# Kernel tuning notes

Hardware: AMD Instinct MI355X
Metric: run time of the kernel (lower is better)

The kernel has to match this reference:

```python
import jax, jax.numpy as jnp
import numpy as np


def setup_inputs() -> dict:
    key = jax.random.key(0)
    ks = jax.random.split(key, 7)
    B, T, E, H, V = 32, 200, 32, 128, 8000
    s = lambda fan: 1.0 / np.sqrt(fan)
    return {
        "x": jax.random.normal(ks[0], (B, T, E), dtype=jnp.float32),
        "Ww": jax.random.normal(ks[1], (H, H), dtype=jnp.float32) * s(H),
        "Wb": jax.random.normal(ks[2], (H,), dtype=jnp.float32) * s(H),
        "Uw": jax.random.normal(ks[3], (H, E), dtype=jnp.float32) * s(E),
        "Ub": jax.random.normal(ks[4], (H,), dtype=jnp.float32) * s(E),
        "Vw": jax.random.normal(ks[5], (V, H), dtype=jnp.float32) * s(H),
        "Vb": jax.random.normal(ks[6], (V,), dtype=jnp.float32) * s(H),
    }


def reference(x, Ww, Wb, Uw, Ub, Vw, Vb):
    # x: [B, T, E]. Elman RNN: h_t = tanh(W h_{t-1} + b_W + U x_t + b_U); out_t = V h_t + b_V
    B = x.shape[0]
    H = Ww.shape[0]
    h0 = jnp.zeros((B, H), dtype=x.dtype)
    # Precompute input projections for all timesteps at once: [T, B, H]
    ux = jnp.einsum('bte,he->tbh', x, Uw) + Ub + Wb

    def step(h, ux_t):
        h = jnp.tanh(h @ Ww.T + ux_t)
        return h, h

    hidden, hs = jax.lax.scan(step, h0, ux)  # hs: [T, B, H]
    # Output projection applied to all hidden states (same math as per-step V)
    out_seq = jnp.einsum('tbh,vh->btv', hs, Vw) + Vb  # [B, T, V]
    return out_seq, hidden
```

## Files before the change

kernel.cpp:

```cpp
#include <hip/hip_runtime.h>
#include <hip/hip_bf16.h>
#include <stdint.h>

typedef short v8s __attribute__((ext_vector_type(8)));
typedef float v4f __attribute__((ext_vector_type(4)));
typedef float v4fv __attribute__((ext_vector_type(4)));

__device__ __forceinline__ float bf2f(short s) {
    unsigned int u = ((unsigned int)(unsigned short)s) << 16;
    float f;
    __builtin_memcpy(&f, &u, 4);
    return f;
}

__device__ __forceinline__ unsigned short f2bf(float f) {
    unsigned int u;
    __builtin_memcpy(&u, &f, 4);
    unsigned int r = (u + 0x7FFFu + ((u >> 16) & 1u)) >> 16;
    return (unsigned short)r;
}

__device__ __forceinline__ float tanh_fast(float z) {
    float e = __expf(2.0f * z);
    return 1.0f - 2.0f / (e + 1.0f);
}

__global__ __launch_bounds__(256) void ux_kernel(
    const float* __restrict__ x, const float* __restrict__ Uw,
    const float* __restrict__ Ub, const float* __restrict__ Wb,
    float* __restrict__ ux) {
    int row = blockIdx.x * 2 + (threadIdx.x >> 7);
    int i = threadIdx.x & 127;
    int b = row & 31, t = row >> 5;
    const float* xr = x + (b * 200 + t) * 32;
    const float* ur = Uw + i * 32;
    float acc = 0.f;
#pragma unroll
    for (int e4 = 0; e4 < 8; ++e4) {
        v4fv xv = *(const v4fv*)(xr + e4 * 4);
        v4fv uv = *(const v4fv*)(ur + e4 * 4);
#pragma unroll
        for (int j = 0; j < 4; ++j) acc = __builtin_fmaf(xv[j], uv[j], acc);
    }
    ux[row * 128 + i] = acc + Ub[i] + Wb[i];
}

__global__ __launch_bounds__(512) void rnn_kernel(
    const float* __restrict__ Ww, const float* __restrict__ ux,
    short* __restrict__ hs, float* __restrict__ hidden_out) {
    __shared__ alignas(16) short h_hi[2][16][136];
    __shared__ alignas(16) short h_lo[2][16][136];
    const int tid = threadIdx.x;
    const int w = tid >> 6;
    const int lane = tid & 63;
    const int q = lane >> 4, c = lane & 15;
    const int b0 = blockIdx.x * 16;
    const int col = 16 * w + c;

    for (int i = tid; i < 2 * 16 * 136; i += 512) {
        ((short*)h_hi)[i] = 0;
        ((short*)h_lo)[i] = 0;
    }

    v8s w_hi[4], w_lo[4];
#pragma unroll
    for (int kb = 0; kb < 4; ++kb) {
        const float* p = Ww + col * 128 + 32 * kb + 8 * q;
#pragma unroll
        for (int j = 0; j < 8; ++j) {
            float v = p[j];
            unsigned short hi = f2bf(v);
            w_hi[kb][j] = (short)hi;
            w_lo[kb][j] = (short)f2bf(v - bf2f((short)hi));
        }
    }

    float uxv[4];
#pragma unroll
    for (int r = 0; r < 4; ++r)
        uxv[r] = ux[(b0 + 4 * q + r) * 128 + col];

    __syncthreads();

    for (int t = 0; t < 200; ++t) {
        float uxn[4];
        int tn = t < 199 ? t + 1 : 199;
#pragma unroll
        for (int r = 0; r < 4; ++r)
            uxn[r] = ux[(tn * 32 + b0 + 4 * q + r) * 128 + col];

        const int rb = t & 1;
        v4f a0 = {0.f, 0.f, 0.f, 0.f}, a1 = a0, a2 = a0;
#pragma unroll
        for (int kb = 0; kb < 4; ++kb) {
            v8s ahi = *(const v8s*)(&h_hi[rb][c][32 * kb + 8 * q]);
            v8s alo = *(const v8s*)(&h_lo[rb][c][32 * kb + 8 * q]);
            a0 = __builtin_amdgcn_mfma_f32_16x16x32_bf16(ahi, w_hi[kb], a0, 0, 0, 0);
            a1 = __builtin_amdgcn_mfma_f32_16x16x32_bf16(ahi, w_lo[kb], a1, 0, 0, 0);
            a2 = __builtin_amdgcn_mfma_f32_16x16x32_bf16(alo, w_hi[kb], a2, 0, 0, 0);
        }

#pragma unroll
        for (int r = 0; r < 4; ++r) {
            float z = ((a0[r] + a1[r]) + a2[r]) + uxv[r];
            float h = tanh_fast(z);
            unsigned short hh = f2bf(h);
            float rem = h - bf2f((short)hh);
            unsigned short hl = f2bf(rem);
            h_hi[rb ^ 1][4 * q + r][col] = (short)hh;
            h_lo[rb ^ 1][4 * q + r][col] = (short)hl;
            hs[((b0 + 4 * q + r) * 200 + t) * 128 + col] = (short)hh;
            if (t == 199) hidden_out[(b0 + 4 * q + r) * 128 + col] = h;
            uxv[r] = uxn[r];
        }
        __syncthreads();
    }
}

__global__ __launch_bounds__(256) void out_kernel(
    const short* __restrict__ hs, const float* __restrict__ Vw,
    const float* __restrict__ Vb, float* __restrict__ out) {
    const int tid = threadIdx.x;
    const int w = tid >> 6;
    const int lane = tid & 63;
    const int q = lane >> 4, c = lane & 15;
    const int v_wave = blockIdx.x * 128 + 32 * w;
    const int bt0 = blockIdx.y * 128;

    v4f acc[2][8];
#pragma unroll
    for (int a = 0; a < 2; ++a)
#pragma unroll
        for (int b = 0; b < 8; ++b) acc[a][b] = (v4f){0.f, 0.f, 0.f, 0.f};

#pragma unroll
    for (int kb = 0; kb < 4; ++kb) {
        v8s afr[2];
#pragma unroll
        for (int vt = 0; vt < 2; ++vt) {
            int vr = v_wave + 16 * vt + c;
            vr = vr < 8000 ? vr : 7999;
            const float* p = Vw + vr * 128 + 32 * kb + 8 * q;
            v4fv p0 = *(const v4fv*)(p);
            v4fv p1 = *(const v4fv*)(p + 4);
#pragma unroll
            for (int j = 0; j < 4; ++j) {
                afr[vt][j] = (short)f2bf(p0[j]);
                afr[vt][4 + j] = (short)f2bf(p1[j]);
            }
        }
#pragma unroll
        for (int nt = 0; nt < 8; ++nt) {
            v8s bfr = *(const v8s*)(hs + (bt0 + 16 * nt + c) * 128 + 32 * kb + 8 * q);
            acc[0][nt] = __builtin_amdgcn_mfma_f32_16x16x32_bf16(afr[0], bfr, acc[0][nt], 0, 0, 0);
            acc[1][nt] = __builtin_amdgcn_mfma_f32_16x16x32_bf16(afr[1], bfr, acc[1][nt], 0, 0, 0);
        }
    }

#pragma unroll
    for (int vt = 0; vt < 2; ++vt) {
        int v4base = v_wave + 16 * vt + 4 * q;
        bool ok = v4base < 8000;
        int vb_idx = ok ? v4base : 0;
        v4fv vbv = *(const v4fv*)(Vb + vb_idx);
#pragma unroll
        for (int nt = 0; nt < 8; ++nt) {
            long bt = bt0 + 16 * nt + c;
            if (ok) {
                v4fv o;
#pragma unroll
                for (int r = 0; r < 4; ++r) o[r] = acc[vt][nt][r] + vbv[r];
                *(v4fv*)(out + bt * 8000 + v4base) = o;
            }
        }
    }
}

extern "C" void kernel_launch(void* const* d_in, const int* in_sizes, int n_in,
                              void* d_out, int out_size, void* d_ws, size_t ws_size,
                              hipStream_t stream) {
    const float* x  = (const float*)d_in[0];
    const float* Ww = (const float*)d_in[1];
    const float* Wb = (const float*)d_in[2];
    const float* Uw = (const float*)d_in[3];
    const float* Ub = (const float*)d_in[4];
    const float* Vw = (const float*)d_in[5];
    const float* Vb = (const float*)d_in[6];
    float* out = (float*)d_out;

    float* ux = (float*)d_ws;
    short* hs = (short*)((char*)d_ws + 819200 * 4);

    ux_kernel<<<3200, 256, 0, stream>>>(x, Uw, Ub, Wb, ux);
    rnn_kernel<<<2, 512, 0, stream>>>(Ww, ux, hs, out + 51200000);
    dim3 g(63, 50);
    out_kernel<<<g, 256, 0, stream>>>(hs, Vw, Vb, out);
}
```

Baseline: 452.0 us.

## Pre-convert Vw to bf16, streamline RNN step, make hidden states time-major

A separate kernel converts Vw to bf16 once, so the output GEMM no longer converts fp32 per block. The recurrent loop is unrolled by two with precomputed LDS offsets and the bias folded into the accumulator init. It also uses cheaper bf16 rounding (round-half-up, truncate for the low part) and an rcp-based tanh. Hidden states are stored time-major so per-step writes are contiguous, and the output kernel remaps indices to match. The final hidden state is rebuilt from the hi+lo split, which slightly changes precision.

```diff
diff --git a/kernel.cpp b/kernel.cpp
--- a/kernel.cpp
+++ b/kernel.cpp
@@ -1,28 +1,29 @@
 #include <hip/hip_runtime.h>
-#include <hip/hip_bf16.h>
 #include <stdint.h>
 
 typedef short v8s __attribute__((ext_vector_type(8)));
 typedef float v4f __attribute__((ext_vector_type(4)));
-typedef float v4fv __attribute__((ext_vector_type(4)));
 
 __device__ __forceinline__ float bf2f(short s) {
     unsigned int u = ((unsigned int)(unsigned short)s) << 16;
-    float f;
-    __builtin_memcpy(&f, &u, 4);
-    return f;
-}
-
-__device__ __forceinline__ unsigned short f2bf(float f) {
-    unsigned int u;
-    __builtin_memcpy(&u, &f, 4);
-    unsigned int r = (u + 0x7FFFu + ((u >> 16) & 1u)) >> 16;
-    return (unsigned short)r;
-}
-
+    float f; __builtin_memcpy(&f, &u, 4); return f;
+}
+__device__ __forceinline__ unsigned short f2bf_rne(float f) {
+    unsigned int u; __builtin_memcpy(&u, &f, 4);
+    return (unsigned short)((u + 0x7FFFu + ((u >> 16) & 1u)) >> 16);
+}
+__device__ __forceinline__ unsigned short f2bf_rhu(float f) {
+    unsigned int u; __builtin_memcpy(&u, &f, 4);
+    return (unsigned short)((u + 0x8000u) >> 16);
+}
+__device__ __forceinline__ unsigned short f2bf_trunc(float f) {
+    unsigned int u; __builtin_memcpy(&u, &f, 4);
+    return (unsigned short)(u >> 16);
+}
 __device__ __forceinline__ float tanh_fast(float z) {
     float e = __expf(2.0f * z);
-    return 1.0f - 2.0f / (e + 1.0f);
+    float r = __builtin_amdgcn_rcpf(e + 1.0f);
+    return __builtin_fmaf(-2.0f, r, 1.0f);
 }
 
 __global__ __launch_bounds__(256) void ux_kernel(
@@ -37,30 +38,39 @@
     float acc = 0.f;
 #pragma unroll
     for (int e4 = 0; e4 < 8; ++e4) {
-        v4fv xv = *(const v4fv*)(xr + e4 * 4);
-        v4fv uv = *(const v4fv*)(ur + e4 * 4);
+        v4f xv = *(const v4f*)(xr + e4 * 4);
+        v4f uv = *(const v4f*)(ur + e4 * 4);
 #pragma unroll
         for (int j = 0; j < 4; ++j) acc = __builtin_fmaf(xv[j], uv[j], acc);
     }
     ux[row * 128 + i] = acc + Ub[i] + Wb[i];
+}
+
+__global__ __launch_bounds__(256) void vwcvt_kernel(
+    const float* __restrict__ Vw, short* __restrict__ vwb) {
+    int i = (blockIdx.x * 256 + threadIdx.x) * 8;
+    v4f p0 = *(const v4f*)(Vw + i);
+    v4f p1 = *(const v4f*)(Vw + i + 4);
+    v8s o;
+#pragma unroll
+    for (int j = 0; j < 4; ++j) {
+        o[j] = (short)f2bf_rne(p0[j]);
+        o[4 + j] = (short)f2bf_rne(p1[j]);
+    }
+    *(v8s*)(vwb + i) = o;
 }
 
 __global__ __launch_bounds__(512) void rnn_kernel(
     const float* __restrict__ Ww, const float* __restrict__ ux,
     short* __restrict__ hs, float* __restrict__ hidden_out) {
-    __shared__ alignas(16) short h_hi[2][16][136];
-    __shared__ alignas(16) short h_lo[2][16][136];
+    __shared__ alignas(16) short hbuf[2 * 2 * 16 * 136];
+    char* lds = (char*)hbuf;
     const int tid = threadIdx.x;
-    const int w = tid >> 6;
-    const int lane = tid & 63;
-    const int q = lane >> 4, c = lane & 15;
+    const int w = tid >> 6, lane = tid & 63, q = lane >> 4, c = lane & 15;
     const int b0 = blockIdx.x * 16;
     const int col = 16 * w + c;
 
-    for (int i = tid; i < 2 * 16 * 136; i += 512) {
-        ((short*)h_hi)[i] = 0;
-        ((short*)h_lo)[i] = 0;
-    }
+    for (int i = tid; i < 1088; i += 512) ((v8s*)hbuf)[i] = (v8s){0, 0, 0, 0, 0, 0, 0, 0};
 
     v8s w_hi[4], w_lo[4];
 #pragma unroll
@@ -69,63 +79,70 @@
 #pragma unroll
         for (int j = 0; j < 8; ++j) {
             float v = p[j];
-            unsigned short hi = f2bf(v);
+            unsigned short hi = f2bf_rne(v);
             w_hi[kb][j] = (short)hi;
-            w_lo[kb][j] = (short)f2bf(v - bf2f((short)hi));
-        }
-    }
-
-    float uxv[4];
-#pragma unroll
-    for (int r = 0; r < 4; ++r)
-        uxv[r] = ux[(b0 + 4 * q + r) * 128 + col];
+            w_lo[kb][j] = (short)f2bf_rne(v - bf2f((short)hi));
+        }
+    }
+
+    const int rd_base = c * 272 + 16 * q;
+    const int wr_base = q * 1088 + col * 2;
+
+    const float* uxp = ux + (b0 + 4 * q) * 128 + col;
+    float uxv0 = uxp[0], uxv1 = uxp[128], uxv2 = uxp[256], uxv3 = uxp[384];
+    uxp += 4096;
+    short* hsp = hs + (b0 + 4 * q) * 128 + col;
 
     __syncthreads();
 
-    for (int t = 0; t < 200; ++t) {
-        float uxn[4];
-        int tn = t < 199 ? t + 1 : 199;
-#pragma unroll
-        for (int r = 0; r < 4; ++r)
-            uxn[r] = ux[(tn * 32 + b0 + 4 * q + r) * 128 + col];
-
-        const int rb = t & 1;
-        v4f a0 = {0.f, 0.f, 0.f, 0.f}, a1 = a0, a2 = a0;
-#pragma unroll
-        for (int kb = 0; kb < 4; ++kb) {
-            v8s ahi = *(const v8s*)(&h_hi[rb][c][32 * kb + 8 * q]);
-            v8s alo = *(const v8s*)(&h_lo[rb][c][32 * kb + 8 * q]);
-            a0 = __builtin_amdgcn_mfma_f32_16x16x32_bf16(ahi, w_hi[kb], a0, 0, 0, 0);
-            a1 = __builtin_amdgcn_mfma_f32_16x16x32_bf16(ahi, w_lo[kb], a1, 0, 0, 0);
-            a2 = __builtin_amdgcn_mfma_f32_16x16x32_bf16(alo, w_hi[kb], a2, 0, 0, 0);
-        }
-
-#pragma unroll
-        for (int r = 0; r < 4; ++r) {
-            float z = ((a0[r] + a1[r]) + a2[r]) + uxv[r];
-            float h = tanh_fast(z);
-            unsigned short hh = f2bf(h);
-            float rem = h - bf2f((short)hh);
-            unsigned short hl = f2bf(rem);
-            h_hi[rb ^ 1][4 * q + r][col] = (short)hh;
-            h_lo[rb ^ 1][4 * q + r][col] = (short)hl;
-            hs[((b0 + 4 * q + r) * 200 + t) * 128 + col] = (short)hh;
-            if (t == 199) hidden_out[(b0 + 4 * q + r) * 128 + col] = h;
-            uxv[r] = uxn[r];
-        }
-        __syncthreads();
+#define RNN_STEP(RBUF, WBUF)                                                        \
+    {                                                                               \
+        float un0 = uxp[0], un1 = uxp[128], un2 = uxp[256], un3 = uxp[384];         \
+        v4f a0 = {uxv0, uxv1, uxv2, uxv3};                                          \
+        v4f a1 = {0.f, 0.f, 0.f, 0.f}, a2 = a1;                                     \
+        _Pragma("unroll") for (int kb = 0; kb < 4; ++kb) {                          \
+            v8s ahi = *(const v8s*)(lds + (RBUF)*8704 + kb * 64 + rd_base);         \
+            v8s alo = *(const v8s*)(lds + (RBUF)*8704 + 4352 + kb * 64 + rd_base);  \
+            a0 = __builtin_amdgcn_mfma_f32_16x16x32_bf16(ahi, w_hi[kb], a0, 0, 0, 0); \
+            a1 = __builtin_amdgcn_mfma_f32_16x16x32_bf16(ahi, w_lo[kb], a1, 0, 0, 0); \
+            a2 = __builtin_amdgcn_mfma_f32_16x16x32_bf16(alo, w_hi[kb], a2, 0, 0, 0); \
+        }                                                                           \
+        _Pragma("unroll") for (int r = 0; r < 4; ++r) {                             \
+            float z = (a0[r] + a1[r]) + a2[r];                                      \
+            float h = tanh_fast(z);                                                 \
+            unsigned short hh = f2bf_rhu(h);                                        \
+            float rem = h - bf2f((short)hh);                                        \
+            unsigned short hl = f2bf_trunc(rem);                                    \
+            *(short*)(lds + (WBUF)*8704 + r * 272 + wr_base) = (short)hh;           \
+            *(short*)(lds + (WBUF)*8704 + 4352 + r * 272 + wr_base) = (short)hl;    \
+            hsp[r * 128] = (short)hh;                                               \
+        }                                                                           \
+        uxv0 = un0; uxv1 = un1; uxv2 = un2; uxv3 = un3;                             \
+        uxp += 4096; hsp += 4096;                                                   \
+        __syncthreads();                                                            \
+    }
+
+    for (int tp = 0; tp < 100; ++tp) {
+        RNN_STEP(0, 1)
+        RNN_STEP(1, 0)
+    }
+#undef RNN_STEP
+
+#pragma unroll
+    for (int r = 0; r < 4; ++r) {
+        short hh = *(short*)(lds + r * 272 + wr_base);
+        short hl = *(short*)(lds + 4352 + r * 272 + wr_base);
+        hidden_out[(b0 + 4 * q + r) * 128 + col] = bf2f(hh) + bf2f(hl);
     }
 }
 
 __global__ __launch_bounds__(256) void out_kernel(
-    const short* __restrict__ hs, const float* __restrict__ Vw,
+    const short* __restrict__ hs, const short* __restrict__ vwb,
     const float* __restrict__ Vb, float* __restrict__ out) {
     const int tid = threadIdx.x;
-    const int w = tid >> 6;
-    const int lane = tid & 63;
-    const int q = lane >> 4, c = lane & 15;
+    const int w = tid >> 6, lane = tid & 63, q = lane >> 4, c = lane & 15;
     const int v_wave = blockIdx.x * 128 + 32 * w;
-    const int bt0 = blockIdx.y * 128;
+    const int n0 = blockIdx.y * 128;
 
     v4f acc[2][8];
 #pragma unroll
@@ -140,18 +157,11 @@
         for (int vt = 0; vt < 2; ++vt) {
             int vr = v_wave + 16 * vt + c;
             vr = vr < 8000 ? vr : 7999;
-            const float* p = Vw + vr * 128 + 32 * kb + 8 * q;
-            v4fv p0 = *(const v4fv*)(p);
-            v4fv p1 = *(const v4fv*)(p + 4);
-#pragma unroll
-            for (int j = 0; j < 4; ++j) {
-                afr[vt][j] = (short)f2bf(p0[j]);
-                afr[vt][4 + j] = (short)f2bf(p1[j]);
-            }
+            afr[vt] = *(const v8s*)(vwb + vr * 128 + 32 * kb + 8 * q);
         }
 #pragma unroll
         for (int nt = 0; nt < 8; ++nt) {
-            v8s bfr = *(const v8s*)(hs + (bt0 + 16 * nt + c) * 128 + 32 * kb + 8 * q);
+            v8s bfr = *(const v8s*)(hs + (n0 + 16 * nt + c) * 128 + 32 * kb + 8 * q);
             acc[0][nt] = __builtin_amdgcn_mfma_f32_16x16x32_bf16(afr[0], bfr, acc[0][nt], 0, 0, 0);
             acc[1][nt] = __builtin_amdgcn_mfma_f32_16x16x32_bf16(afr[1], bfr, acc[1][nt], 0, 0, 0);
         }
@@ -161,16 +171,17 @@
     for (int vt = 0; vt < 2; ++vt) {
         int v4base = v_wave + 16 * vt + 4 * q;
         bool ok = v4base < 8000;
-        int vb_idx = ok ? v4base : 0;
-        v4fv vbv = *(const v4fv*)(Vb + vb_idx);
+        v4f vbv = *(const v4f*)(Vb + (ok ? v4base : 0));
 #pragma unroll
         for (int nt = 0; nt < 8; ++nt) {
-            long bt = bt0 + 16 * nt + c;
+            int n = n0 + 16 * nt + c;
+            int t = n >> 5, b = n & 31;
+            unsigned int off = (unsigned int)(b * 200 + t) * 8000u + (unsigned int)v4base;
             if (ok) {
-                v4fv o;
+                v4f o;
 #pragma unroll
                 for (int r = 0; r < 4; ++r) o[r] = acc[vt][nt][r] + vbv[r];
-                *(v4fv*)(out + bt * 8000 + v4base) = o;
+                *(v4f*)(out + (size_t)off) = o;
             }
         }
     }
@@ -189,10 +200,12 @@
     float* out = (float*)d_out;
 
     float* ux = (float*)d_ws;
-    short* hs = (short*)((char*)d_ws + 819200 * 4);
+    short* hs = (short*)((char*)d_ws + 3276800);
+    short* vwb = (short*)d_ws;
 
     ux_kernel<<<3200, 256, 0, stream>>>(x, Uw, Ub, Wb, ux);
     rnn_kernel<<<2, 512, 0, stream>>>(Ww, ux, hs, out + 51200000);
+    vwcvt_kernel<<<500, 256, 0, stream>>>(Vw, vwb);
     dim3 g(63, 50);
-    out_kernel<<<g, 256, 0, stream>>>(hs, Vw, Vb, out);
-}
+    out_kernel<<<g, 256, 0, stream>>>(hs, vwb, Vb, out);
+}
```

After: 405.0 us. 10.4% less time.
